# Kernel tuning notes

Measured on AMD Instinct MI355X. Metric: run time of the kernel, lower is better.

## Reference

```python
import jax, jax.numpy as jnp
import numpy as np

COST_CLASS = 1.0
COST_BBOX = 1.0
COST_GIOU = 1.0
NUM_TGT_PER_IMG = 100  # sizes[b] for every image (equal-size, padded-batch style)


def box_cxcywh_to_xyxy(b):
    cx, cy, w, h = jnp.split(b, 4, axis=-1)
    return jnp.concatenate([cx - 0.5 * w, cy - 0.5 * h, cx + 0.5 * w, cy + 0.5 * h], axis=-1)


def generalized_box_iou(b1, b2):
    # b1: [N,4], b2: [M,4] in xyxy -> [N,M]
    area1 = (b1[:, 2] - b1[:, 0]) * (b1[:, 3] - b1[:, 1])
    area2 = (b2[:, 2] - b2[:, 0]) * (b2[:, 3] - b2[:, 1])
    lt = jnp.maximum(b1[:, None, :2], b2[None, :, :2])
    rb = jnp.minimum(b1[:, None, 2:], b2[None, :, 2:])
    wh = jnp.clip(rb - lt, 0.0)
    inter = wh[..., 0] * wh[..., 1]
    union = area1[:, None] + area2[None, :] - inter
    iou = inter / union
    lt_e = jnp.minimum(b1[:, None, :2], b2[None, :, :2])
    rb_e = jnp.maximum(b1[:, None, 2:], b2[None, :, 2:])
    wh_e = jnp.clip(rb_e - lt_e, 0.0)
    area_e = wh_e[..., 0] * wh_e[..., 1]
    return iou - (area_e - union) / area_e


def build_cost_matrix(logits, pred_boxes, tgt_labels, tgt_boxes):
    B, Q, C = logits.shape
    out_prob = jax.nn.sigmoid(logits).reshape(B * Q, C)        # [BQ, C]
    out_bbox = pred_boxes.reshape(B * Q, 4)                     # [BQ, 4]
    tgt_ids = tgt_labels.reshape(-1)                            # [BT]
    tgt_bbox = tgt_boxes.reshape(-1, 4)                         # [BT, 4]
    cost_class = -out_prob[:, tgt_ids]                          # [BQ, BT]
    cost_bbox = jnp.sum(jnp.abs(out_bbox[:, None, :] - tgt_bbox[None, :, :]), axis=-1)  # L1 cdist
    cost_giou = -generalized_box_iou(box_cxcywh_to_xyxy(out_bbox), box_cxcywh_to_xyxy(tgt_bbox))
    cost = COST_BBOX * cost_bbox + COST_CLASS * cost_class + COST_GIOU * cost_giou
    return cost.reshape(B, Q, -1)                               # [B, Q, B*T]


def greedy_match(cost, curr_targets):
    # Faithful to _greedy_matcher: iteratively pick the globally smallest-cost
    # unmatched (row, col) pair among columns < curr_targets. Equivalent to the
    # stable-sorted flat scan (argmin breaks ties at lowest flat index, matching
    # the stable ascending sort).
    Q, Ttot = cost.shape
    col_ok = jnp.arange(Ttot) < curr_targets
    c0 = jnp.where(col_ok[None, :], cost, jnp.inf)
    num_match = min(Q, curr_targets)

    def step(c, _):
        idx = jnp.argmin(c.reshape(-1))
        r = idx // Ttot
        col = idx % Ttot
        c = c.at[r, :].set(jnp.inf).at[:, col].set(jnp.inf)
        return c, (r.astype(jnp.int32), col.astype(jnp.int32))

    _, (rows, cols) = jax.lax.scan(step, c0, None, length=num_match)
    return rows, cols


def setup_inputs() -> dict:
    key = jax.random.key(0)
    k1, k2, k3, k4, k5, k6 = jax.random.split(key, 6)
    B, Q, C, T = 16, 900, 91, NUM_TGT_PER_IMG
    logits = jax.random.normal(k1, (B, Q, C), dtype=jnp.float32)
    pb_cxcy = jax.random.uniform(k2, (B, Q, 2), dtype=jnp.float32)
    pb_wh = jax.random.uniform(k3, (B, Q, 2), dtype=jnp.float32, minval=0.05, maxval=0.5)
    pred_boxes = jnp.concatenate([pb_cxcy, pb_wh], axis=-1)
    tgt_labels = jax.random.randint(k4, (B, T), 0, C)
    tb_cxcy = jax.random.uniform(k5, (B, T, 2), dtype=jnp.float32)
    tb_wh = jax.random.uniform(k6, (B, T, 2), dtype=jnp.float32, minval=0.05, maxval=0.5)
    tgt_boxes = jnp.concatenate([tb_cxcy, tb_wh], axis=-1)
    return {"logits": logits, "pred_boxes": pred_boxes, "tgt_labels": tgt_labels, "tgt_boxes": tgt_boxes}


def reference(logits, pred_boxes, tgt_labels, tgt_boxes):
    cost = build_cost_matrix(logits, pred_boxes, tgt_labels, tgt_boxes)  # [B, Q, B*T]
    rows, cols = jax.vmap(lambda c: greedy_match(c, NUM_TGT_PER_IMG))(cost)
    return cost, rows, cols
```

## Files before the change

kernel.cpp:

```cpp
#include <hip/hip_runtime.h>
#include <math.h>

#define BB 16
#define QQ 900
#define CC 91
#define TT 100
#define BT (BB * TT)
#define NTHREADS 256
#define TILE 15
#define NBLK_PER_IMG (QQ / TILE)
#define NSLOT 15
#define WSCOLS 128
#define PENDK 8

__device__ __forceinline__ unsigned ordkey(float f) {
    unsigned u = __float_as_uint(f);
    return (u & 0x80000000u) ? ~u : (u | 0x80000000u);
}

__device__ __forceinline__ unsigned long long u64min(unsigned long long a, unsigned long long b) {
    return a < b ? a : b;
}
__device__ __forceinline__ unsigned long long u64max(unsigned long long a, unsigned long long b) {
    return a > b ? a : b;
}

__device__ __forceinline__ unsigned long long packkrc(unsigned key, int row, int col) {
    return ((unsigned long long)key << 21) | ((unsigned long long)row << 11) | (unsigned)col;
}

__device__ __forceinline__ unsigned long long rdlane64(unsigned long long v, int l) {
    unsigned lo = (unsigned)__builtin_amdgcn_readlane((int)(unsigned)v, l);
    unsigned hi = (unsigned)__builtin_amdgcn_readlane((int)(unsigned)(v >> 32), l);
    return ((unsigned long long)hi << 32) | lo;
}

__global__ __launch_bounds__(NTHREADS) void cost_kernel(
    const float* __restrict__ logits,
    const float* __restrict__ pred,
    const int*   __restrict__ tlab,
    const float* __restrict__ tbox,
    float*       __restrict__ cost,
    unsigned long long* __restrict__ colmin)
{
    const int b  = blockIdx.x / NBLK_PER_IMG;
    const int tb = blockIdx.x % NBLK_PER_IMG;
    const int r0 = tb * TILE;

    __shared__ float s_tx[BT], s_ty[BT], s_tz[BT], s_tw[BT];
    __shared__ int   s_lab[BT];
    __shared__ float s_sig[TILE][CC];
    __shared__ float s_row[TILE][8];

    for (int j = threadIdx.x; j < BT; j += NTHREADS) {
        float4 t = *(const float4*)(tbox + (size_t)j * 4);
        s_tx[j] = t.x; s_ty[j] = t.y; s_tz[j] = t.z; s_tw[j] = t.w;
        s_lab[j] = tlab[j];
    }
    for (int u = threadIdx.x; u < TILE * CC; u += NTHREADS) {
        int r = u / CC, c = u % CC;
        float x = logits[((size_t)(b * QQ + r0 + r)) * CC + c];
        s_sig[r][c] = 1.0f / (1.0f + expf(-x));
    }
    if (threadIdx.x < TILE) {
        int r = threadIdx.x;
        const float4 p = *(const float4*)(pred + ((size_t)(b * QQ + r0 + r)) * 4);
        s_row[r][0] = p.x; s_row[r][1] = p.y; s_row[r][2] = p.z; s_row[r][3] = p.w;
        s_row[r][4] = p.x - 0.5f * p.z;
        s_row[r][5] = p.y - 0.5f * p.w;
        s_row[r][6] = p.x + 0.5f * p.z;
        s_row[r][7] = p.y + 0.5f * p.w;
    }
    __syncthreads();

    unsigned long long bestc = ~0ULL;

    for (int r = 0; r < TILE; ++r) {
        const float px  = s_row[r][0], py  = s_row[r][1], pz  = s_row[r][2], pw  = s_row[r][3];
        const float p_x0 = s_row[r][4], p_y0 = s_row[r][5], p_x1 = s_row[r][6], p_y1 = s_row[r][7];
        const float area1 = (p_x1 - p_x0) * (p_y1 - p_y0);
        float* crow = cost + ((size_t)(b * QQ + r0 + r)) * BT;

        for (int j = threadIdx.x; j < BT; j += NTHREADS) {
            float tx = s_tx[j], ty = s_ty[j], tz = s_tz[j], tw = s_tw[j];
            float cclass = -s_sig[r][s_lab[j]];
            float cbbox = ((fabsf(px - tx) + fabsf(py - ty)) + fabsf(pz - tz)) + fabsf(pw - tw);

            float t_x0 = tx - 0.5f * tz, t_y0 = ty - 0.5f * tw;
            float t_x1 = tx + 0.5f * tz, t_y1 = ty + 0.5f * tw;
            float area2 = (t_x1 - t_x0) * (t_y1 - t_y0);

            float ltx = fmaxf(p_x0, t_x0), lty = fmaxf(p_y0, t_y0);
            float rbx = fminf(p_x1, t_x1), rby = fminf(p_y1, t_y1);
            float iw = fmaxf(rbx - ltx, 0.0f), ih = fmaxf(rby - lty, 0.0f);
            float inter = iw * ih;
            float uni = (area1 + area2) - inter;
            float iou = inter / uni;

            float ex0 = fminf(p_x0, t_x0), ey0 = fminf(p_y0, t_y0);
            float ex1 = fmaxf(p_x1, t_x1), ey1 = fmaxf(p_y1, t_y1);
            float ew = fmaxf(ex1 - ex0, 0.0f), eh = fmaxf(ey1 - ey0, 0.0f);
            float ae = ew * eh;
            float giou = iou - (ae - uni) / ae;

            float v = (cbbox + cclass) + (-giou);
            crow[j] = v;
            if (j < TT) bestc = u64min(bestc, packkrc(ordkey(v), r0 + r, j));
        }
    }

    if (threadIdx.x < TT)
        atomicMin(colmin + (size_t)b * WSCOLS + threadIdx.x, bestc);
}

__global__ __launch_bounds__(64, 1) void greedy_kernel(
    const float* __restrict__ cost,
    const unsigned long long* __restrict__ colmin,
    float*       __restrict__ rows_out,
    float*       __restrict__ cols_out)
{
    const int b = blockIdx.x;
    const int lane = threadIdx.x;
    const float* cb = cost + (size_t)b * QQ * BT;

    unsigned long long va = colmin[(size_t)b * WSCOLS + lane];
    unsigned long long vb = (lane < TT - 64)
                          ? colmin[(size_t)b * WSCOLS + 64 + lane] : ~0ULL;

    #pragma unroll
    for (int k = 2; k <= 128; k <<= 1) {
        #pragma unroll
        for (int j = k >> 1; j > 0; j >>= 1) {
            if (j == 64) {
                unsigned long long lo = u64min(va, vb);
                unsigned long long hi = va ^ vb ^ lo;
                va = lo; vb = hi;
            } else {
                unsigned long long pa = __shfl_xor(va, j, 64);
                bool ta = ((lane & j) == 0) == ((lane & k) == 0);
                va = ta ? u64min(va, pa) : u64max(va, pa);
                unsigned long long pb = __shfl_xor(vb, j, 64);
                int ib = lane + 64;
                bool tb_ = ((ib & j) == 0) == ((ib & k) == 0);
                vb = tb_ ? u64min(vb, pb) : u64max(vb, pb);
            }
        }
    }

    unsigned rowok = (lane < 4) ? 0x7FFFu : 0x3FFFu;
    unsigned long long pend[PENDK];
    #pragma unroll
    for (int t = 0; t < PENDK; ++t) pend[t] = ~0ULL;
    unsigned long long pmin = ~0ULL;

    int p = 0;
    int match = 0;
    while (match < TT) {
        unsigned long long s = (p < 64) ? rdlane64(va, p)
                             : (p < 128) ? rdlane64(vb, p - 64) : ~0ULL;
        bool fromPend = pmin < s;
        unsigned long long e = fromPend ? pmin : s;

        const int rstar = (int)((e >> 11) & 0x3FF);
        const int cstar = (int)(e & 0x7FF);

        bool alive = __ballot((lane == (rstar & 63)) && ((rowok >> (rstar >> 6)) & 1u)) != 0ULL;

        if (fromPend) {
            bool removed = false;
            #pragma unroll
            for (int t = 0; t < PENDK; ++t) {
                if (!removed && pend[t] == e) { pend[t] = ~0ULL; removed = true; }
            }
            pmin = ~0ULL;
            #pragma unroll
            for (int t = 0; t < PENDK; ++t) pmin = u64min(pmin, pend[t]);
        } else {
            ++p;
        }

        if (alive) {
            if (lane == 0) {
                rows_out[b * TT + match] = (float)rstar;
                cols_out[b * TT + match] = (float)cstar;
            }
            if (lane == (rstar & 63)) rowok &= ~(1u << (rstar >> 6));
            ++match;
        } else {
            unsigned long long best = ~0ULL;
            #pragma unroll
            for (int i = 0; i < NSLOT; ++i) {
                if ((rowok >> i) & 1u) {
                    const int r = i * 64 + lane;
                    float v = cb[(size_t)r * BT + cstar];
                    best = u64min(best, packkrc(ordkey(v), r, cstar));
                }
            }
            #pragma unroll
            for (int off = 1; off < 64; off <<= 1)
                best = u64min(best, __shfl_xor(best, off, 64));

            bool placed = false;
            #pragma unroll
            for (int t = 0; t < PENDK; ++t) {
                if (!placed && pend[t] == ~0ULL) { pend[t] = best; placed = true; }
            }
            pmin = u64min(pmin, best);
        }
    }
}

extern "C" void kernel_launch(void* const* d_in, const int* in_sizes, int n_in,
                              void* d_out, int out_size, void* d_ws, size_t ws_size,
                              hipStream_t stream) {
    const float* logits = (const float*)d_in[0];
    const float* pred   = (const float*)d_in[1];
    const int*   tlab   = (const int*)d_in[2];
    const float* tbox   = (const float*)d_in[3];

    float* out = (float*)d_out;
    float* cost = out;
    float* rows = out + (size_t)BB * QQ * BT;
    float* cols = rows + (size_t)BB * TT;

    unsigned long long* colmin = (unsigned long long*)d_ws;

    hipMemsetAsync(d_ws, 0xFF, (size_t)BB * WSCOLS * sizeof(unsigned long long), stream);

    cost_kernel<<<BB * NBLK_PER_IMG, NTHREADS, 0, stream>>>(logits, pred, tlab, tbox, cost, colmin);
    greedy_kernel<<<BB, 64, 0, stream>>>(cost, colmin, rows, cols);
}
```

Measured before the change: 204.7 us.

## Batch-accept greedy matches per wavefront step and use nontemporal cost stores

The greedy matcher now accepts a whole run of consecutive sorted column minima in one step. It finds the first entry that conflicts (dead row, duplicate row, or beaten by a pending candidate) using LDS atomics and a ballot, instead of walking one entry per iteration with readlane. Row liveness moves to an LDS byte array. The cost kernel packs target boxes as float4 in LDS and writes the large cost matrix with nontemporal stores to avoid polluting the cache. This adds LDS traffic and explicit waitcnt barriers per step, and the pending-list logic is more intricate.

```diff
diff --git a/kernel.cpp b/kernel.cpp
--- a/kernel.cpp
+++ b/kernel.cpp
@@ -47,14 +47,13 @@
     const int tb = blockIdx.x % NBLK_PER_IMG;
     const int r0 = tb * TILE;
 
-    __shared__ float s_tx[BT], s_ty[BT], s_tz[BT], s_tw[BT];
-    __shared__ int   s_lab[BT];
-    __shared__ float s_sig[TILE][CC];
-    __shared__ float s_row[TILE][8];
+    __shared__ float4 s_t[BT];
+    __shared__ int    s_lab[BT];
+    __shared__ float  s_sig[TILE][CC];
+    __shared__ float  s_row[TILE][8];
 
     for (int j = threadIdx.x; j < BT; j += NTHREADS) {
-        float4 t = *(const float4*)(tbox + (size_t)j * 4);
-        s_tx[j] = t.x; s_ty[j] = t.y; s_tz[j] = t.z; s_tw[j] = t.w;
+        s_t[j] = *(const float4*)(tbox + (size_t)j * 4);
         s_lab[j] = tlab[j];
     }
     for (int u = threadIdx.x; u < TILE * CC; u += NTHREADS) {
@@ -82,12 +81,12 @@
         float* crow = cost + ((size_t)(b * QQ + r0 + r)) * BT;
 
         for (int j = threadIdx.x; j < BT; j += NTHREADS) {
-            float tx = s_tx[j], ty = s_ty[j], tz = s_tz[j], tw = s_tw[j];
+            float4 t = s_t[j];
             float cclass = -s_sig[r][s_lab[j]];
-            float cbbox = ((fabsf(px - tx) + fabsf(py - ty)) + fabsf(pz - tz)) + fabsf(pw - tw);
-
-            float t_x0 = tx - 0.5f * tz, t_y0 = ty - 0.5f * tw;
-            float t_x1 = tx + 0.5f * tz, t_y1 = ty + 0.5f * tw;
+            float cbbox = ((fabsf(px - t.x) + fabsf(py - t.y)) + fabsf(pz - t.z)) + fabsf(pw - t.w);
+
+            float t_x0 = t.x - 0.5f * t.z, t_y0 = t.y - 0.5f * t.w;
+            float t_x1 = t.x + 0.5f * t.z, t_y1 = t.y + 0.5f * t.w;
             float area2 = (t_x1 - t_x0) * (t_y1 - t_y0);
 
             float ltx = fmaxf(p_x0, t_x0), lty = fmaxf(p_y0, t_y0);
@@ -104,7 +103,7 @@
             float giou = iou - (ae - uni) / ae;
 
             float v = (cbbox + cclass) + (-giou);
-            crow[j] = v;
+            __builtin_nontemporal_store(v, &crow[j]);
             if (j < TT) bestc = u64min(bestc, packkrc(ordkey(v), r0 + r, j));
         }
     }
@@ -122,6 +121,13 @@
     const int b = blockIdx.x;
     const int lane = threadIdx.x;
     const float* cb = cost + (size_t)b * QQ * BT;
+
+    __shared__ unsigned s_first[1024];
+    __shared__ unsigned s_dead32[256];
+    unsigned char* s_dead = (unsigned char*)s_dead32;
+
+    #pragma unroll
+    for (int kk = 0; kk < 4; ++kk) s_dead32[lane + kk * 64] = 0u;
 
     unsigned long long va = colmin[(size_t)b * WSCOLS + lane];
     unsigned long long vb = (lane < TT - 64)
@@ -147,65 +153,131 @@
         }
     }
 
-    unsigned rowok = (lane < 4) ? 0x7FFFu : 0x3FFFu;
+    const int rA = (int)((va >> 11) & 0x3FF);
+    const int cA = (int)(va & 0x7FF);
+    const int rB = (int)((vb >> 11) & 0x3FF);
+    const int cB = (int)(vb & 0x7FF);
+
     unsigned long long pend[PENDK];
     #pragma unroll
     for (int t = 0; t < PENDK; ++t) pend[t] = ~0ULL;
     unsigned long long pmin = ~0ULL;
 
-    int p = 0;
-    int match = 0;
-    while (match < TT) {
-        unsigned long long s = (p < 64) ? rdlane64(va, p)
-                             : (p < 128) ? rdlane64(vb, p - 64) : ~0ULL;
-        bool fromPend = pmin < s;
-        unsigned long long e = fromPend ? pmin : s;
-
-        const int rstar = (int)((e >> 11) & 0x3FF);
-        const int cstar = (int)(e & 0x7FF);
-
-        bool alive = __ballot((lane == (rstar & 63)) && ((rowok >> (rstar >> 6)) & 1u)) != 0ULL;
-
-        if (fromPend) {
+    int cur = 0;
+    int m = 0;
+
+    while (m < TT) {
+        __asm__ volatile("s_waitcnt lgkmcnt(0)" ::: "memory");
+
+        #pragma unroll
+        for (int kk = 0; kk < 16; ++kk) s_first[lane + kk * 64] = 0xFFFFFFFFu;
+
+        bool dA = s_dead[rA] != 0;
+        bool dB = s_dead[rB] != 0;
+        __asm__ volatile("s_waitcnt lgkmcnt(0)" ::: "memory");
+
+        bool inA = (lane >= cur) && !dA;
+        bool inB = ((64 + lane) >= cur) && !dB;
+        if (inA) atomicMin(&s_first[rA], (unsigned)lane);
+        if (inB) atomicMin(&s_first[rB], (unsigned)(64 + lane));
+        __asm__ volatile("s_waitcnt lgkmcnt(0)" ::: "memory");
+
+        bool dupA = inA && (s_first[rA] < (unsigned)lane);
+        bool dupB = inB && (s_first[rB] < (unsigned)(64 + lane));
+
+        bool evA = (lane >= cur)        && (dA || dupA || (pmin < va));
+        bool evB = ((64 + lane) >= cur) && (dB || dupB || (pmin < vb));
+        unsigned long long mA = __ballot(evA);
+        unsigned long long mB = __ballot(evB);
+        int k = mA ? (int)__ffsll(mA) - 1
+              : (mB ? 64 + (int)__ffsll(mB) - 1 : 128);
+
+        int n = k - cur;
+        if (n > TT - m) n = TT - m;
+
+        if (n > 0) {
+            int iA = lane - cur;
+            if (iA >= 0 && iA < n) {
+                rows_out[b * TT + m + iA] = (float)rA;
+                cols_out[b * TT + m + iA] = (float)cA;
+                s_dead[rA] = 1;
+            }
+            int iB = 64 + lane - cur;
+            if (iB >= 0 && iB < n) {
+                rows_out[b * TT + m + iB] = (float)rB;
+                cols_out[b * TT + m + iB] = (float)cB;
+                s_dead[rB] = 1;
+            }
+            m += n;
+            cur += n;
+            if (m >= TT) break;
+        }
+
+        unsigned long long ecur = (cur < 64) ? rdlane64(va, cur)
+                                : (cur < 128) ? rdlane64(vb, cur - 64) : ~0ULL;
+        __asm__ volatile("s_waitcnt lgkmcnt(0)" ::: "memory");
+
+        if (pmin < ecur) {
+            unsigned long long e = pmin;
             bool removed = false;
             #pragma unroll
-            for (int t = 0; t < PENDK; ++t) {
+            for (int t = 0; t < PENDK; ++t)
                 if (!removed && pend[t] == e) { pend[t] = ~0ULL; removed = true; }
-            }
             pmin = ~0ULL;
             #pragma unroll
             for (int t = 0; t < PENDK; ++t) pmin = u64min(pmin, pend[t]);
+
+            int re = (int)((e >> 11) & 0x3FF);
+            int ce = (int)(e & 0x7FF);
+            bool alive = (s_dead[re] == 0);
+            if (alive) {
+                if (lane == 0) {
+                    rows_out[b * TT + m] = (float)re;
+                    cols_out[b * TT + m] = (float)ce;
+                    s_dead[re] = 1;
+                }
+                ++m;
+            } else {
+                unsigned long long best = ~0ULL;
+                #pragma unroll
+                for (int i = 0; i < NSLOT; ++i) {
+                    int r = i * 64 + lane;
+                    bool ok = (r < QQ) && (s_dead[r] == 0);
+                    if (ok) {
+                        float v = cb[(size_t)r * BT + ce];
+                        best = u64min(best, packkrc(ordkey(v), r, ce));
+                    }
+                }
+                #pragma unroll
+                for (int off = 1; off < 64; off <<= 1)
+                    best = u64min(best, __shfl_xor(best, off, 64));
+                bool placed = false;
+                #pragma unroll
+                for (int t = 0; t < PENDK; ++t)
+                    if (!placed && pend[t] == ~0ULL) { pend[t] = best; placed = true; }
+                pmin = u64min(pmin, best);
+            }
         } else {
-            ++p;
-        }
-
-        if (alive) {
-            if (lane == 0) {
-                rows_out[b * TT + match] = (float)rstar;
-                cols_out[b * TT + match] = (float)cstar;
-            }
-            if (lane == (rstar & 63)) rowok &= ~(1u << (rstar >> 6));
-            ++match;
-        } else {
+            int cc = (int)(ecur & 0x7FF);
             unsigned long long best = ~0ULL;
             #pragma unroll
             for (int i = 0; i < NSLOT; ++i) {
-                if ((rowok >> i) & 1u) {
-                    const int r = i * 64 + lane;
-                    float v = cb[(size_t)r * BT + cstar];
-                    best = u64min(best, packkrc(ordkey(v), r, cstar));
+                int r = i * 64 + lane;
+                bool ok = (r < QQ) && (s_dead[r] == 0);
+                if (ok) {
+                    float v = cb[(size_t)r * BT + cc];
+                    best = u64min(best, packkrc(ordkey(v), r, cc));
                 }
             }
             #pragma unroll
             for (int off = 1; off < 64; off <<= 1)
                 best = u64min(best, __shfl_xor(best, off, 64));
-
             bool placed = false;
             #pragma unroll
-            for (int t = 0; t < PENDK; ++t) {
+            for (int t = 0; t < PENDK; ++t)
                 if (!placed && pend[t] == ~0ULL) { pend[t] = best; placed = true; }
-            }
             pmin = u64min(pmin, best);
+            ++cur;
         }
     }
 }
```

Measured after the change: 217.4 us. 1.06x slower.
